# Optimization experiments

Measured on AMD Instinct MI355X. Metric: run time of the kernel, lower is better.

## Reference

```python
import math
import jax, jax.numpy as jnp
import numpy as np

B, N, D, H = 2, 8192, 1024, 16


def setup_inputs() -> dict:
    key = jax.random.key(0)
    k1, k2, k3, k4 = jax.random.split(key, 4)
    s = 1.0 / math.sqrt(D)
    return {
        "x": jax.random.normal(k1, (B, N, D), dtype=jnp.float32),
        "W_qk": jax.random.normal(k2, (D, D), dtype=jnp.float32) * s,
        "W_v": jax.random.normal(k3, (D, D), dtype=jnp.float32) * s,
        "W_out": jax.random.normal(k4, (D, D), dtype=jnp.float32) * s,
        "tau": jnp.ones((H, 1, 1), dtype=jnp.float32),
    }


def reference(x, W_qk, W_v, W_out, tau):
    b, n, d = x.shape
    h = H
    dh = d // h
    # QK / V projections (no bias), then to channel-major (B, H, dh, N)
    qk = (x @ W_qk).transpose(0, 2, 1).reshape(b, h, dh, n)
    v = (x @ W_v).transpose(0, 2, 1).reshape(b, h, dh, n)
    # Cross-channel Gram matrix over tokens: (B, H, dh, dh)
    dot = jnp.einsum('bhcn,bhdn->bhcd', qk, qk)
    q2 = jnp.sum(qk * qk, axis=-1)  # (B, H, dh)
    # Negative squared Euclidean distance between channel vectors
    logits = (2.0 * dot - q2[:, :, :, None] - q2[:, :, None, :]) / math.sqrt(max(n, 1))
    logits = logits * tau[None, ...]
    attn = jax.nn.softmax(logits, axis=-1)  # (B, H, dh, dh)
    w = jnp.einsum('bhcd,bhdn->bhcn', attn, v)  # (B, H, dh, N)
    out = w.reshape(b, d, n).transpose(0, 2, 1) @ W_out  # (B, N, D)
    return out
```

## Files before the change

kernel.cpp:

```cpp
#include <hip/hip_runtime.h>
#include <hip/hip_bf16.h>
#include <cstdint>
#include <cstddef>

typedef __bf16 v8bf __attribute__((ext_vector_type(8)));
typedef float  v4f  __attribute__((ext_vector_type(4)));

__device__ __forceinline__ unsigned short f2bf(float f) {
    unsigned int u = __float_as_uint(f);
    u += 0x7fffu + ((u >> 16) & 1u);
    return (unsigned short)(u >> 16);
}

__device__ __forceinline__ void gload_lds16(const unsigned short* g, unsigned short* l) {
    __builtin_amdgcn_global_load_lds(
        (const __attribute__((address_space(1))) unsigned int*)(uintptr_t)g,
        (__attribute__((address_space(3))) unsigned int*)(uintptr_t)l, 16, 0, 0);
}

template<int WRITE_BF16>
__global__ __launch_bounds__(256, 2) void gemm_bt(
    const unsigned short* __restrict__ A,
    const unsigned short* __restrict__ BT,
    void* __restrict__ C,
    int K, int lda, int ldb, int ldc,
    size_t sAz, size_t sBz, size_t sCz,
    int nBlk, int mPerXcd)
{
    __shared__ unsigned short sA[128 * 32];
    __shared__ unsigned short sB[128 * 32];

    const int id = blockIdx.x;
    const int xcd = id & 7;
    int s = id >> 3;
    const int perXcd = mPerXcd * nBlk;
    const int z = s / perXcd;
    s -= z * perXcd;
    const int mB = xcd * mPerXcd + s / nBlk;
    const int nB = s - (s / nBlk) * nBlk;

    const unsigned short* Ab = A + (size_t)z * sAz;
    const unsigned short* Bb = BT + (size_t)z * sBz;

    const int tid  = threadIdx.x;
    const int wv   = tid >> 6;
    const int lane = tid & 63;
    const int quad = lane >> 4;
    const int l16  = lane & 15;
    const size_t bm = (size_t)mB * 128;
    const size_t bn = (size_t)nB * 128;
    const int wm = (wv >> 1) * 64;
    const int wn = (wv & 1) * 64;

    const int ro = tid >> 2;
    const int ko = (((tid & 3) ^ (ro & 3)) << 3);

    const unsigned short* aptr0 = Ab + (bm + ro)      * (size_t)lda + ko;
    const unsigned short* aptr1 = Ab + (bm + ro + 64) * (size_t)lda + ko;
    const unsigned short* bptr0 = Bb + (bn + ro)      * (size_t)ldb + ko;
    const unsigned short* bptr1 = Bb + (bn + ro + 64) * (size_t)ldb + ko;

    unsigned short* sA0 = &sA[wv * 512];
    unsigned short* sA1 = &sA[2048 + wv * 512];
    unsigned short* sB0 = &sB[wv * 512];
    unsigned short* sB1 = &sB[2048 + wv * 512];

    const int sslot = ((quad ^ (l16 & 3)) << 3);

    v4f acc[4][4] = {};

    for (int k0 = 0; k0 < K; k0 += 32) {
        gload_lds16(aptr0 + k0, sA0);
        gload_lds16(aptr1 + k0, sA1);
        gload_lds16(bptr0 + k0, sB0);
        gload_lds16(bptr1 + k0, sB1);
        __syncthreads();

        v8bf af[4], bfr[4];
        #pragma unroll
        for (int t = 0; t < 4; t++) {
            af[t]  = *(const v8bf*)&sA[(size_t)(wm + t * 16 + l16) * 32 + sslot];
            bfr[t] = *(const v8bf*)&sB[(size_t)(wn + t * 16 + l16) * 32 + sslot];
        }

        #pragma unroll
        for (int ti = 0; ti < 4; ti++)
            #pragma unroll
            for (int tj = 0; tj < 4; tj++)
                acc[ti][tj] = __builtin_amdgcn_mfma_f32_16x16x32_bf16(
                    af[ti], bfr[tj], acc[ti][tj], 0, 0, 0);
        __syncthreads();
    }

    if (WRITE_BF16) {
        unsigned short* Cb = (unsigned short*)C + (size_t)z * sCz;
        #pragma unroll
        for (int ti = 0; ti < 4; ti++) {
            const size_t row0 = bm + wm + ti * 16 + quad * 4;
            #pragma unroll
            for (int tj = 0; tj < 4; tj++) {
                const size_t col = bn + wn + tj * 16 + l16;
                #pragma unroll
                for (int r = 0; r < 4; r++)
                    Cb[(row0 + r) * (size_t)ldc + col] = f2bf(acc[ti][tj][r]);
            }
        }
    } else {
        float* Cb = (float*)C + (size_t)z * sCz;
        #pragma unroll
        for (int ti = 0; ti < 4; ti++) {
            const size_t row0 = bm + wm + ti * 16 + quad * 4;
            #pragma unroll
            for (int tj = 0; tj < 4; tj++) {
                const size_t col = bn + wn + tj * 16 + l16;
                #pragma unroll
                for (int r = 0; r < 4; r++)
                    Cb[(row0 + r) * (size_t)ldc + col] = acc[ti][tj][r];
            }
        }
    }
}

#define MFMA_QUAD(MH, NH)                                                     \
    do {                                                                      \
        __builtin_amdgcn_s_setprio(1);                                        \
        _Pragma("unroll")                                                     \
        for (int mi = 0; mi < 4; ++mi) {                                      \
            _Pragma("unroll")                                                 \
            for (int ni = 0; ni < 2; ++ni) {                                  \
                acc[(MH)*4 + mi][(NH)*2 + ni] =                               \
                    __builtin_amdgcn_mfma_f32_16x16x32_bf16(                  \
                        aF[mi][0], bF[NH][ni][0],                             \
                        acc[(MH)*4 + mi][(NH)*2 + ni], 0, 0, 0);              \
                acc[(MH)*4 + mi][(NH)*2 + ni] =                               \
                    __builtin_amdgcn_mfma_f32_16x16x32_bf16(                  \
                        aF[mi][1], bF[NH][ni][1],                             \
                        acc[(MH)*4 + mi][(NH)*2 + ni], 0, 0, 0);              \
            }                                                                 \
        }                                                                     \
        __builtin_amdgcn_s_setprio(0);                                        \
    } while (0)

template<int WRITE_BF16>
__global__ __launch_bounds__(512, 2) void gemm256_bt(
    const unsigned short* __restrict__ A,
    const unsigned short* __restrict__ BT,
    void* __restrict__ C,
    int K, int lda, int ldb, int ldc,
    size_t sAz, size_t sBz, size_t sCz,
    int nBlk, int mPerXcd)
{
    __shared__ unsigned short sm[65536];

    const int id = blockIdx.x;
    const int xcd = id & 7;
    int s = id >> 3;
    const int perXcd = mPerXcd * nBlk;
    const int z = s / perXcd;
    s -= z * perXcd;
    const int mB = xcd * mPerXcd + s / nBlk;
    const int nB = s - (s / nBlk) * nBlk;

    const unsigned short* Ab = A + (size_t)z * sAz;
    const unsigned short* Bb = BT + (size_t)z * sBz;

    const int tid  = threadIdx.x;
    const int wv   = tid >> 6;
    const int lane = tid & 63;
    const int quad = lane >> 4;
    const int l16  = lane & 15;
    const int wm   = wv >> 2;
    const int wn   = wv & 3;

    const size_t bm = (size_t)mB * 256;
    const size_t bn = (size_t)nB * 256;

    const int r0   = tid >> 3;
    const int slog = (tid & 7) ^ (r0 & 7);
    const unsigned short* aP = Ab + (bm + r0) * (size_t)lda + slog * 8;
    const unsigned short* bP = Bb + (bn + r0) * (size_t)ldb + slog * 8;

    const int stA = wv * 512;

    const int soff0 = (quad ^ (l16 & 7)) * 8;
    const int arow0 = (wm * 64 + l16) * 64 + soff0;
    const int brow0 = (wn * 32 + l16) * 64 + soff0;

    v4f  acc[8][4] = {};
    v8bf aF[4][2];
    v8bf bF[2][2][2];

    const int NT = K >> 6;

    {
        gload_lds16(aP,                sm + stA);
        gload_lds16(aP + 64 * lda,     sm + stA + 4096);
        gload_lds16(bP,                sm + 32768 + stA);
        gload_lds16(bP + 64 * ldb,     sm + 32768 + stA + 4096);
        gload_lds16(bP + 128 * ldb,    sm + 32768 + 8192 + stA);
        gload_lds16(bP + 192 * ldb,    sm + 32768 + 8192 + stA + 4096);
        gload_lds16(aP + 128 * lda,    sm + 8192 + stA);
        gload_lds16(aP + 192 * lda,    sm + 8192 + stA + 4096);
        if (NT > 1) {
            gload_lds16(aP + 64,                 sm + 16384 + stA);
            gload_lds16(aP + 64 * lda + 64,      sm + 16384 + stA + 4096);
            gload_lds16(bP + 64,                 sm + 32768 + 16384 + stA);
            gload_lds16(bP + 64 * ldb + 64,      sm + 32768 + 16384 + stA + 4096);
            gload_lds16(bP + 128 * ldb + 64,     sm + 32768 + 16384 + 8192 + stA);
            gload_lds16(bP + 192 * ldb + 64,     sm + 32768 + 16384 + 8192 + stA + 4096);
            asm volatile("s_waitcnt vmcnt(6)" ::: "memory");
        } else {
            asm volatile("s_waitcnt vmcnt(0)" ::: "memory");
        }
        __builtin_amdgcn_s_barrier();
    }

    for (int t = 0; t < NT; ++t) {
        const int p = t & 1;
        const unsigned short* sa = sm + p * 16384;
        const unsigned short* sb = sm + 32768 + p * 16384;
        unsigned short* dq = sm + (p ^ 1) * 16384;
        unsigned short* dp = sm + p * 16384;
        const int kk1 = (t + 1) * 64;
        const int kk2 = (t + 2) * 64;

        #pragma unroll
        for (int mi = 0; mi < 4; ++mi) {
            aF[mi][0] = *(const v8bf*)(sa + (arow0 + mi * 1024));
            aF[mi][1] = *(const v8bf*)(sa + ((arow0 + mi * 1024) ^ 32));
        }
        #pragma unroll
        for (int ni = 0; ni < 2; ++ni) {
            bF[0][ni][0] = *(const v8bf*)(sb + (brow0 + ni * 1024));
            bF[0][ni][1] = *(const v8bf*)(sb + ((brow0 + ni * 1024) ^ 32));
        }
        if (t + 1 < NT) {
            gload_lds16(aP + 128 * lda + kk1, dq + 8192 + stA);
            gload_lds16(aP + 192 * lda + kk1, dq + 8192 + stA + 4096);
        }
        __builtin_amdgcn_s_barrier();
        asm volatile("s_waitcnt lgkmcnt(0)" ::: "memory");
        MFMA_QUAD(0, 0);
        __builtin_amdgcn_s_barrier();

        #pragma unroll
        for (int ni = 0; ni < 2; ++ni) {
            bF[1][ni][0] = *(const v8bf*)(sb + 8192 + (brow0 + ni * 1024));
            bF[1][ni][1] = *(const v8bf*)(sb + 8192 + ((brow0 + ni * 1024) ^ 32));
        }
        if (t + 2 < NT) {
            gload_lds16(aP + kk2,            dp + stA);
            gload_lds16(aP + 64 * lda + kk2, dp + stA + 4096);
        }
        __builtin_amdgcn_s_barrier();
        asm volatile("s_waitcnt lgkmcnt(0)" ::: "memory");
        MFMA_QUAD(0, 1);
        __builtin_amdgcn_s_barrier();

        #pragma unroll
        for (int mi = 0; mi < 4; ++mi) {
            aF[mi][0] = *(const v8bf*)(sa + 8192 + (arow0 + mi * 1024));
            aF[mi][1] = *(const v8bf*)(sa + 8192 + ((arow0 + mi * 1024) ^ 32));
        }
        if (t + 2 < NT) {
            gload_lds16(bP + kk2,            dp + 32768 + stA);
            gload_lds16(bP + 64 * ldb + kk2, dp + 32768 + stA + 4096);
        }
        __builtin_amdgcn_s_barrier();
        asm volatile("s_waitcnt lgkmcnt(0)" ::: "memory");
        MFMA_QUAD(1, 1);
        __builtin_amdgcn_s_barrier();

        if (t + 2 < NT) {
            gload_lds16(bP + 128 * ldb + kk2, dp + 32768 + 8192 + stA);
            gload_lds16(bP + 192 * ldb + kk2, dp + 32768 + 8192 + stA + 4096);
            asm volatile("s_waitcnt vmcnt(6)" ::: "memory");
        } else {
            asm volatile("s_waitcnt vmcnt(0)" ::: "memory");
        }
        __builtin_amdgcn_s_barrier();
        MFMA_QUAD(1, 0);
        __builtin_amdgcn_s_barrier();
    }

    if (WRITE_BF16) {
        unsigned short* Cb = (unsigned short*)C + (size_t)z * sCz;
        #pragma unroll
        for (int mh = 0; mh < 2; ++mh)
            #pragma unroll
            for (int mi = 0; mi < 4; ++mi) {
                const size_t row0 = bm + mh * 128 + wm * 64 + mi * 16 + quad * 4;
                #pragma unroll
                for (int nh = 0; nh < 2; ++nh)
                    #pragma unroll
                    for (int ni = 0; ni < 2; ++ni) {
                        const size_t col = bn + nh * 128 + wn * 32 + ni * 16 + l16;
                        #pragma unroll
                        for (int r = 0; r < 4; ++r)
                            Cb[(row0 + r) * (size_t)ldc + col] =
                                f2bf(acc[mh * 4 + mi][nh * 2 + ni][r]);
                    }
            }
    } else {
        float* Cb = (float*)C + (size_t)z * sCz;
        #pragma unroll
        for (int mh = 0; mh < 2; ++mh)
            #pragma unroll
            for (int mi = 0; mi < 4; ++mi) {
                const size_t row0 = bm + mh * 128 + wm * 64 + mi * 16 + quad * 4;
                #pragma unroll
                for (int nh = 0; nh < 2; ++nh)
                    #pragma unroll
                    for (int ni = 0; ni < 2; ++ni) {
                        const size_t col = bn + nh * 128 + wn * 32 + ni * 16 + l16;
                        #pragma unroll
                        for (int r = 0; r < 4; ++r)
                            Cb[(row0 + r) * (size_t)ldc + col] =
                                acc[mh * 4 + mi][nh * 2 + ni][r];
                    }
            }
    }
}
#undef MFMA_QUAD

__global__ __launch_bounds__(256) void gram_kernel(
    const unsigned short* __restrict__ qk,
    float* __restrict__ partial)
{
    const int bh = blockIdx.x;
    const int split = blockIdx.y;
    const int b = bh >> 4, h = bh & 15;
    const unsigned short* base = qk + (size_t)b * 8192 * 1024 + (size_t)h * 64;
    const int n0 = split * 512;

    __shared__ unsigned short sMT[64 * 136];
    const int tid = threadIdx.x;
    const int wv = tid >> 6, lane = tid & 63, quad = lane >> 4, l16 = lane & 15;

    uint4 pre[4];
    #pragma unroll
    for (int i = 0; i < 4; i++) {
        const int ch = tid + i * 256, tok = ch >> 3, co = (ch & 7) << 3;
        pre[i] = *(const uint4*)(base + (size_t)(n0 + tok) * 1024 + co);
    }

    v4f acc[4] = {};

    for (int chunk = 0; chunk < 4; chunk++) {
        __syncthreads();
        #pragma unroll
        for (int i = 0; i < 4; i++) {
            const int ch = tid + i * 256, tok = ch >> 3, co = (ch & 7) << 3;
            union { uint4 v; unsigned short s8[8]; } u; u.v = pre[i];
            #pragma unroll
            for (int j = 0; j < 8; j++)
                sMT[(size_t)(co + j) * 136 + tok] = u.s8[j];
        }
        __syncthreads();

        if (chunk < 3) {
            const int nb = n0 + (chunk + 1) * 128;
            #pragma unroll
            for (int i = 0; i < 4; i++) {
                const int ch = tid + i * 256, tok = ch >> 3, co = (ch & 7) << 3;
                pre[i] = *(const uint4*)(base + (size_t)(nb + tok) * 1024 + co);
            }
        }

        #pragma unroll
        for (int ks = 0; ks < 4; ks++) {
            const int kb = ks * 32 + quad * 8;
            const v8bf a = *(const v8bf*)&sMT[(size_t)(16 * wv + l16) * 136 + kb];
            #pragma unroll
            for (int t = 0; t < 4; t++) {
                const v8bf bb = *(const v8bf*)&sMT[(size_t)(t * 16 + l16) * 136 + kb];
                acc[t] = __builtin_amdgcn_mfma_f32_16x16x32_bf16(a, bb, acc[t], 0, 0, 0);
            }
        }
    }

    float* outp = partial + ((size_t)split * 32 + bh) * 4096;
    #pragma unroll
    for (int t = 0; t < 4; t++)
        #pragma unroll
        for (int r = 0; r < 4; r++)
            outp[(size_t)(16 * wv + quad * 4 + r) * 64 + t * 16 + l16] = acc[t][r];
}

__global__ __launch_bounds__(256) void softmax_kernel(
    const float* __restrict__ partial,
    const float* __restrict__ tau,
    float* __restrict__ attnT)
{
    const int gw = (int)((blockIdx.x * 256 + threadIdx.x) >> 6);
    const int d = threadIdx.x & 63;
    const int bh = gw >> 6;
    const int c = gw & 63;
    const int h = bh & 15;

    float cd = 0.f, cc = 0.f, dd = 0.f;
    #pragma unroll
    for (int s = 0; s < 16; s++) {
        const float* p = partial + ((size_t)s * 32 + bh) * 4096;
        cd += p[c * 64 + d];
        cc += p[c * 65];
        dd += p[d * 65];
    }
    const float INV_SQRT_N = 0.011048543456039806f;
    const float logit = (2.f * cd - cc - dd) * INV_SQRT_N * tau[h];

    float m = logit;
    #pragma unroll
    for (int off = 32; off > 0; off >>= 1) m = fmaxf(m, __shfl_xor(m, off, 64));
    const float e = __expf(logit - m);
    float sum = e;
    #pragma unroll
    for (int off = 32; off > 0; off >>= 1) sum += __shfl_xor(sum, off, 64);

    attnT[(size_t)bh * 4096 + d * 64 + c] = e / sum;
}

__global__ __launch_bounds__(256) void wefft_kernel(
    const float* __restrict__ attnT,
    const float* __restrict__ Wout,
    unsigned short* __restrict__ weffT)
{
    const int bh = blockIdx.x;
    const int jg = blockIdx.y;
    const int b = bh >> 4, h = bh & 15;

    __shared__ float sAttT[64][65];
    __shared__ float sW[64][65];
    const int tid = threadIdx.x;
    const float* ap = attnT + (size_t)bh * 4096;
    const float* wp = Wout + (size_t)(h * 64) * 1024 + jg * 64;
    for (int i = tid; i < 4096; i += 256) {
        const int r = i >> 6, q = i & 63;
        sAttT[r][q] = ap[i];
        sW[r][q] = wp[(size_t)r * 1024 + q];
    }
    __syncthreads();

    const int dd0 = (tid >> 4) << 2;
    const int j0  = (tid & 15) << 2;
    float acc[4][4] = {};
    for (int cc = 0; cc < 64; cc++) {
        float av[4], wvv[4];
        #pragma unroll
        for (int i = 0; i < 4; i++) av[i] = sAttT[dd0 + i][cc];
        #pragma unroll
        for (int i = 0; i < 4; i++) wvv[i] = sW[cc][j0 + i];
        #pragma unroll
        for (int i = 0; i < 4; i++)
            #pragma unroll
            for (int j = 0; j < 4; j++)
                acc[i][j] += av[i] * wvv[j];
    }

    unsigned short* op = weffT + ((size_t)b * 1024 + jg * 64) * 1024 + h * 64;
    #pragma unroll
    for (int i = 0; i < 4; i++)
        #pragma unroll
        for (int j = 0; j < 4; j++)
            op[(size_t)(j0 + j) * 1024 + dd0 + i] = f2bf(acc[i][j]);
}

__global__ __launch_bounds__(256) void cvt_all_kernel(
    const float* __restrict__ x, const float* __restrict__ Wv,
    const float* __restrict__ Wqk,
    unsigned short* __restrict__ xb, unsigned short* __restrict__ wvb,
    unsigned short* __restrict__ wqkT)
{
    const int bid = blockIdx.x;
    if (bid < 17408) {
        const float* src = (bid < 16384) ? x : Wv;
        unsigned short* dst = (bid < 16384) ? xb : wvb;
        const size_t blk = (bid < 16384) ? bid : (bid - 16384);
        const size_t i = (blk * 256 + threadIdx.x) * 4;
        const float4 v = *(const float4*)(src + i);
        ushort4 o;
        o.x = f2bf(v.x); o.y = f2bf(v.y); o.z = f2bf(v.z); o.w = f2bf(v.w);
        *(ushort4*)(dst + i) = o;
    } else {
        const int t = bid - 17408;
        const int n0 = (t & 31) * 32, k0 = (t >> 5) * 32;
        __shared__ float sT[32][33];
        const int tx = threadIdx.x & 31, ty = threadIdx.x >> 5;
        #pragma unroll
        for (int i = ty; i < 32; i += 8)
            sT[i][tx] = Wqk[(size_t)(k0 + i) * 1024 + n0 + tx];
        __syncthreads();
        #pragma unroll
        for (int i = ty; i < 32; i += 8)
            wqkT[(size_t)(n0 + i) * 1024 + k0 + tx] = f2bf(sT[tx][i]);
    }
}

extern "C" void kernel_launch(void* const* d_in, const int* in_sizes, int n_in,
                              void* d_out, int out_size, void* d_ws, size_t ws_size,
                              hipStream_t stream)
{
    (void)in_sizes; (void)n_in; (void)out_size; (void)ws_size;
    const float* x    = (const float*)d_in[0];
    const float* Wqk  = (const float*)d_in[1];
    const float* Wv   = (const float*)d_in[2];
    const float* Wout = (const float*)d_in[3];
    const float* tau  = (const float*)d_in[4];

    unsigned short* xb     = (unsigned short*)d_ws;
    unsigned short* wqkT   = xb + (size_t)16384 * 1024;
    unsigned short* wvb    = wqkT + (size_t)1024 * 1024;
    unsigned short* qk     = wvb + (size_t)1024 * 1024;
    float*          partial= (float*)(qk + (size_t)16384 * 1024);
    float*          attnT  = partial + (size_t)16 * 32 * 4096;
    unsigned short* weffT  = (unsigned short*)(attnT + (size_t)32 * 4096);
    unsigned short* wfoldT = weffT + (size_t)2 * 1024 * 1024;

    cvt_all_kernel<<<18432, 256, 0, stream>>>(x, Wv, Wqk, xb, wvb, wqkT);

    gemm256_bt<1><<<256, 512, 0, stream>>>(
        xb, wqkT, (void*)qk, 1024, 1024, 1024, 1024, 0, 0, 0, 4, 8);

    gram_kernel<<<dim3(32, 16), 256, 0, stream>>>(qk, partial);
    softmax_kernel<<<512, 256, 0, stream>>>(partial, tau, attnT);
    wefft_kernel<<<dim3(32, 16), 256, 0, stream>>>(attnT, Wout, weffT);

    gemm_bt<1><<<128, 256, 0, stream>>>(
        weffT, wvb, (void*)wfoldT, 1024, 1024, 1024, 1024,
        (size_t)1024 * 1024, 0, (size_t)1024 * 1024, 8, 1);

    gemm256_bt<0><<<256, 512, 0, stream>>>(
        xb, wfoldT, d_out, 1024, 1024, 1024, 1024,
        (size_t)8192 * 1024, (size_t)1024 * 1024, (size_t)8192 * 1024, 4, 4);
}
```

Before: 261.6 us.

## Emit QK projection channel-major so Gram kernel loads tiles directly into LDS

The QK projection GEMM now computes W_qk^T · x^T, producing a channel-major qkT (1024 x 16384) buffer, with a swapBig flag that remaps the block index so the large dimension still spreads across XCDs. The Gram kernel then pulls its whole 64x512 tile straight into swizzled LDS with global_load_lds, replacing the register prefetch, scalar transposing LDS stores and chunked double-sync loop. This targets the transpose overhead and LDS bank traffic in the Gram stage. In exchange the GEMM writes its output with a long row stride, and the Gram kernel uses 64 KB of LDS per block.

Result: faster. 253.0 us (-3.3%).

```diff
diff --git a/kernel.cpp b/kernel.cpp
--- a/kernel.cpp
+++ b/kernel.cpp
@@ -148,7 +148,7 @@
     void* __restrict__ C,
     int K, int lda, int ldb, int ldc,
     size_t sAz, size_t sBz, size_t sCz,
-    int nBlk, int mPerXcd)
+    int nBlk, int mPerXcd, int swapBig)
 {
     __shared__ unsigned short sm[65536];
 
@@ -158,8 +158,10 @@
     const int perXcd = mPerXcd * nBlk;
     const int z = s / perXcd;
     s -= z * perXcd;
-    const int mB = xcd * mPerXcd + s / nBlk;
-    const int nB = s - (s / nBlk) * nBlk;
+    const int bigB   = xcd * mPerXcd + s / nBlk;
+    const int smallB = s - (s / nBlk) * nBlk;
+    const int mB = swapBig ? smallB : bigB;
+    const int nB = swapBig ? bigB : smallB;
 
     const unsigned short* Ab = A + (size_t)z * sAz;
     const unsigned short* Bb = BT + (size_t)z * sBz;
@@ -323,59 +325,41 @@
 }
 #undef MFMA_QUAD
 
-__global__ __launch_bounds__(256) void gram_kernel(
-    const unsigned short* __restrict__ qk,
+__global__ __launch_bounds__(256, 2) void gram_kernel(
+    const unsigned short* __restrict__ qkT,
     float* __restrict__ partial)
 {
     const int bh = blockIdx.x;
     const int split = blockIdx.y;
     const int b = bh >> 4, h = bh & 15;
-    const unsigned short* base = qk + (size_t)b * 8192 * 1024 + (size_t)h * 64;
-    const int n0 = split * 512;
-
-    __shared__ unsigned short sMT[64 * 136];
+    const unsigned short* base =
+        qkT + (size_t)(h * 64) * 16384 + (size_t)b * 8192 + (size_t)split * 512;
+
+    __shared__ unsigned short sM[64 * 512];
     const int tid = threadIdx.x;
     const int wv = tid >> 6, lane = tid & 63, quad = lane >> 4, l16 = lane & 15;
 
-    uint4 pre[4];
-    #pragma unroll
-    for (int i = 0; i < 4; i++) {
-        const int ch = tid + i * 256, tok = ch >> 3, co = (ch & 7) << 3;
-        pre[i] = *(const uint4*)(base + (size_t)(n0 + tok) * 1024 + co);
-    }
+    #pragma unroll
+    for (int i = 0; i < 16; i++) {
+        const int row = i * 4 + wv;
+        const int lo  = (lane & 56) | ((lane & 7) ^ (row & 7));
+        gload_lds16(base + (size_t)row * 16384 + lo * 8,
+                    sM + (size_t)i * 2048 + wv * 512);
+    }
+    __syncthreads();
 
     v4f acc[4] = {};
-
-    for (int chunk = 0; chunk < 4; chunk++) {
-        __syncthreads();
-        #pragma unroll
-        for (int i = 0; i < 4; i++) {
-            const int ch = tid + i * 256, tok = ch >> 3, co = (ch & 7) << 3;
-            union { uint4 v; unsigned short s8[8]; } u; u.v = pre[i];
-            #pragma unroll
-            for (int j = 0; j < 8; j++)
-                sMT[(size_t)(co + j) * 136 + tok] = u.s8[j];
-        }
-        __syncthreads();
-
-        if (chunk < 3) {
-            const int nb = n0 + (chunk + 1) * 128;
-            #pragma unroll
-            for (int i = 0; i < 4; i++) {
-                const int ch = tid + i * 256, tok = ch >> 3, co = (ch & 7) << 3;
-                pre[i] = *(const uint4*)(base + (size_t)(nb + tok) * 1024 + co);
-            }
-        }
-
-        #pragma unroll
-        for (int ks = 0; ks < 4; ks++) {
-            const int kb = ks * 32 + quad * 8;
-            const v8bf a = *(const v8bf*)&sMT[(size_t)(16 * wv + l16) * 136 + kb];
-            #pragma unroll
-            for (int t = 0; t < 4; t++) {
-                const v8bf bb = *(const v8bf*)&sMT[(size_t)(t * 16 + l16) * 136 + kb];
-                acc[t] = __builtin_amdgcn_mfma_f32_16x16x32_bf16(a, bb, acc[t], 0, 0, 0);
-            }
+    const int cha = 16 * wv + l16;
+
+    #pragma unroll
+    for (int ks = 0; ks < 16; ks++) {
+        const int lg = ks * 4 + quad;
+        const int so = ((lg & 56) | ((lg & 7) ^ (l16 & 7))) * 8;
+        const v8bf a = *(const v8bf*)&sM[(size_t)cha * 512 + so];
+        #pragma unroll
+        for (int t = 0; t < 4; t++) {
+            const v8bf bb = *(const v8bf*)&sM[(size_t)(t * 16 + l16) * 512 + so];
+            acc[t] = __builtin_amdgcn_mfma_f32_16x16x32_bf16(a, bb, acc[t], 0, 0, 0);
         }
     }
 
@@ -510,8 +494,8 @@
     unsigned short* xb     = (unsigned short*)d_ws;
     unsigned short* wqkT   = xb + (size_t)16384 * 1024;
     unsigned short* wvb    = wqkT + (size_t)1024 * 1024;
-    unsigned short* qk     = wvb + (size_t)1024 * 1024;
-    float*          partial= (float*)(qk + (size_t)16384 * 1024);
+    unsigned short* qkT    = wvb + (size_t)1024 * 1024;
+    float*          partial= (float*)(qkT + (size_t)16384 * 1024);
     float*          attnT  = partial + (size_t)16 * 32 * 4096;
     unsigned short* weffT  = (unsigned short*)(attnT + (size_t)32 * 4096);
     unsigned short* wfoldT = weffT + (size_t)2 * 1024 * 1024;
@@ -519,9 +503,9 @@
     cvt_all_kernel<<<18432, 256, 0, stream>>>(x, Wv, Wqk, xb, wvb, wqkT);
 
     gemm256_bt<1><<<256, 512, 0, stream>>>(
-        xb, wqkT, (void*)qk, 1024, 1024, 1024, 1024, 0, 0, 0, 4, 8);
-
-    gram_kernel<<<dim3(32, 16), 256, 0, stream>>>(qk, partial);
+        wqkT, xb, (void*)qkT, 1024, 1024, 1024, 16384, 0, 0, 0, 4, 8, 1);
+
+    gram_kernel<<<dim3(32, 16), 256, 0, stream>>>(qkT, partial);
     softmax_kernel<<<512, 256, 0, stream>>>(partial, tau, attnT);
     wefft_kernel<<<dim3(32, 16), 256, 0, stream>>>(attnT, Wout, weffT);
 
@@ -531,5 +515,5 @@
 
     gemm256_bt<0><<<256, 512, 0, stream>>>(
         xb, wfoldT, d_out, 1024, 1024, 1024, 1024,
-        (size_t)8192 * 1024, (size_t)1024 * 1024, (size_t)8192 * 1024, 4, 4);
-}
+        (size_t)8192 * 1024, (size_t)1024 * 1024, (size_t)8192 * 1024, 4, 4, 0);
+}
```
